# Performance work log

Measured on AMD Instinct MI355X. Metric: run time of the kernel, lower is better.

Reference implementation:

```python
import jax, jax.numpy as jnp
import numpy as np

N_HEAD = 16
N_EMBD = 1024
B, T = 4, 1024


def setup_inputs() -> dict:
    key = jax.random.key(0)
    ks = jax.random.split(key, 8)
    hs = N_EMBD // N_HEAD
    x = jax.random.normal(ks[0], (B, T, N_EMBD), dtype=jnp.float32)
    # previous-layer attention load per token, ~O(1/T) like a softmax column mean
    refractory_state = jax.random.uniform(ks[1], (B, T), dtype=jnp.float32) / T
    s_attn = 1.0 / np.sqrt(N_EMBD)
    W_attn = jax.random.normal(ks[2], (N_EMBD, 3 * N_EMBD), dtype=jnp.float32) * s_attn
    b_attn = jnp.zeros((3 * N_EMBD,), dtype=jnp.float32)
    W_proj = jax.random.normal(ks[3], (N_EMBD, N_EMBD), dtype=jnp.float32) * s_attn
    b_proj = jnp.zeros((N_EMBD,), dtype=jnp.float32)
    # learnable LIF params, init per module (lif_mode='refractory')
    threshold = jnp.full((N_HEAD,), 0.01, dtype=jnp.float32)
    leak = jnp.full((N_HEAD,), 2.0, dtype=jnp.float32)
    steepness = jnp.full((N_HEAD,), 2.0, dtype=jnp.float32)
    ref_strength = jnp.full((N_HEAD,), -2.0, dtype=jnp.float32)
    cross_w = jnp.full((N_HEAD,), -2.0, dtype=jnp.float32)
    return {
        "x": x, "refractory_state": refractory_state,
        "W_attn": W_attn, "b_attn": b_attn,
        "W_proj": W_proj, "b_proj": b_proj,
        "threshold": threshold, "leak": leak, "steepness": steepness,
        "ref_strength": ref_strength, "cross_w": cross_w,
    }


def reference(x, refractory_state, W_attn, b_attn, W_proj, b_proj,
              threshold, leak, steepness, ref_strength, cross_w):
    Bq, Tq, C = x.shape
    H = N_HEAD
    hs = C // H
    qkv = x @ W_attn + b_attn                     # [B,T,3C]
    q, k, v = jnp.split(qkv, 3, axis=-1)
    q = q.reshape(Bq, Tq, H, hs).transpose(0, 2, 1, 3)  # [B,H,T,hs]
    k = k.reshape(Bq, Tq, H, hs).transpose(0, 2, 1, 3)
    v = v.reshape(Bq, Tq, H, hs).transpose(0, 2, 1, 3)

    att = jnp.einsum('bhqd,bhkd->bhqk', q, k) * (1.0 / jnp.sqrt(jnp.asarray(hs, x.dtype)))
    causal = jnp.tril(jnp.ones((Tq, Tq), dtype=bool))
    att = jnp.where(causal[None, None], att, -jnp.inf)
    probs = jax.nn.softmax(att, axis=-1)          # [B,H,T,T]

    thr = (jnp.abs(threshold) * 0.1)[None, :, None, None]
    lk = jax.nn.sigmoid(leak)[None, :, None, None]
    st = jax.nn.softplus(steepness)[None, :, None, None]
    # refractory: column load over queries + cross-layer load
    column_load = probs.mean(axis=-2, keepdims=True)          # [B,H,1,T]
    eff_thr = thr + jax.nn.softplus(ref_strength)[None, :, None, None] * column_load
    eff_thr = eff_thr + jax.nn.sigmoid(cross_w)[None, :, None, None] * refractory_state[:, None, None, :]

    fire = jax.nn.sigmoid(st * (probs - eff_thr))
    lif_w = fire + lk * (1.0 - fire)
    mod = probs * lif_w
    mod = mod / (mod.sum(axis=-1, keepdims=True) + 1e-8)
    new_refractory = mod.mean(axis=1).mean(axis=-2)           # [B,T]

    y = jnp.einsum('bhqk,bhkd->bhqd', mod, v)
    y = y.transpose(0, 2, 1, 3).reshape(Bq, Tq, C)
    y = y @ W_proj + b_proj
    return y, new_refractory
```

## Files before the change

kernel.cpp:

```cpp
#include <hip/hip_runtime.h>
#include <math.h>

#define B_  4
#define T_  1024
#define C_  1024
#define H_  16
#define HS_ 64
#define K2E 0.1803368801f
#define LOG2E 1.44269504f

typedef _Float16 f16;
typedef _Float16 f16x8 __attribute__((ext_vector_type(8)));
typedef _Float16 f16x4 __attribute__((ext_vector_type(4)));
typedef float f32x4 __attribute__((ext_vector_type(4)));

#define MFMA16(a,b,c) __builtin_amdgcn_mfma_f32_16x16x32_f16(a,b,c,0,0,0)
#define EXP2(x) __builtin_amdgcn_exp2f(x)
#define RCP(x)  __builtin_amdgcn_rcpf(x)

#define PSTRIDE_BH 557056

__device__ __forceinline__ float qsum_(float v){
    v += __shfl_xor(v,1,64); v += __shfl_xor(v,2,64);
    v += __shfl_xor(v,4,64); v += __shfl_xor(v,8,64);
    return v;
}
__device__ __forceinline__ float sigmoidf_(float x){ return 1.0f/(1.0f + __expf(-x)); }
__device__ __forceinline__ float softplusf_(float x){ return fmaxf(x, 0.0f) + log1pf(__expf(-fabsf(x))); }

__device__ __forceinline__ void gload_lds16(const f16* g, f16* l){
    __builtin_amdgcn_global_load_lds(
        (__attribute__((address_space(1))) void*)(void*)g,
        (__attribute__((address_space(3))) void*)(void*)l, 16, 0, 0);
}

__global__ __launch_bounds__(256) void prep_k(
    const float* __restrict__ x, const float* __restrict__ Wa,
    const float* __restrict__ Wp,
    f16* __restrict__ x_h, f16* __restrict__ WaT, f16* __restrict__ WpT,
    float* __restrict__ zbase)
{
    __shared__ float tl[32][33];
    const int bid = blockIdx.x, tid = threadIdx.x;
    if (bid < 2048){
        int i = bid*256 + tid;
        const float4* p = (const float4*)x + (size_t)i*2;
        float4 a = p[0], b = p[1];
        f16x8 o;
        o[0]=(f16)a.x; o[1]=(f16)a.y; o[2]=(f16)a.z; o[3]=(f16)a.w;
        o[4]=(f16)b.x; o[5]=(f16)b.y; o[6]=(f16)b.z; o[7]=(f16)b.w;
        *((f16x8*)x_h + i) = o;
    } else if (bid < 5120){
        int t = bid - 2048;
        int n0 = (t % 96)*32, k0 = (t / 96)*32;
        const int c = tid & 31, r4 = tid >> 5;
        #pragma unroll
        for (int i=0;i<4;i++){ int r = r4*4+i; tl[r][c] = Wa[(size_t)(k0+r)*3072 + n0 + c]; }
        __syncthreads();
        #pragma unroll
        for (int i=0;i<4;i++){ int r = r4*4+i; WaT[(size_t)(n0+r)*1024 + k0 + c] = (f16)tl[c][r]; }
    } else if (bid < 6144){
        int t = bid - 5120;
        int n0 = (t & 31)*32, k0 = (t >> 5)*32;
        const int c = tid & 31, r4 = tid >> 5;
        #pragma unroll
        for (int i=0;i<4;i++){ int r = r4*4+i; tl[r][c] = Wp[(size_t)(k0+r)*1024 + n0 + c]; }
        __syncthreads();
        #pragma unroll
        for (int i=0;i<4;i++){ int r = r4*4+i; WpT[(size_t)(n0+r)*1024 + k0 + c] = (f16)tl[c][r]; }
    } else {
        int idx = (bid - 6144)*256 + tid;
        float4 z; z.x=0.f; z.y=0.f; z.z=0.f; z.w=0.f;
        ((float4*)zbase)[idx] = z;
    }
}

#define CT_STRIDE  132
#define CTV_STRIDE 136
__global__ __launch_bounds__(256) void gemm_qkv_k(
    const f16* __restrict__ A, const f16* __restrict__ Bt,
    const float* __restrict__ bias,
    f16* __restrict__ Qh, f16* __restrict__ Kh, f16* __restrict__ Vt)
{
    __shared__ __align__(16) f16 smem[17408];
    const int tid = threadIdx.x;
    const int lane = tid & 63, wave = tid >> 6;
    const int lx = lane & 15, quad = lane >> 4;
    const int wm = wave & 1, wn = wave >> 1;
    const int lin = blockIdx.y*24 + blockIdx.x;
    const int nb  = (lin & 7)*96 + (lin >> 3);
    const int m0 = (nb/24)*128, n0 = (nb%24)*128;
    const f16* Ap = A  + (size_t)m0*1024;
    const f16* Bp = Bt + (size_t)n0*1024;
    f32x4 acc[4][4];
    #pragma unroll
    for (int i=0;i<4;i++){
        #pragma unroll
        for (int j=0;j<4;j++){ acc[i][j][0]=0.f;acc[i][j][1]=0.f;acc[i][j][2]=0.f;acc[i][j][3]=0.f; }
    }
#define GQ_STAGE(BUF, KT) { \
    const int k0s = (KT)*32; \
    for (int i=0;i<2;i++){ int c=i*4+wave; \
        gload_lds16(Ap + (size_t)(c*16+lx)*1024 + k0s + quad*8, &smem[(BUF) + c*512]); \
        gload_lds16(Bp + (size_t)(c*16+lx)*1024 + k0s + quad*8, &smem[(BUF) + 4096 + c*512]); } }
#define GQ_COMP(BUF) { \
    f16x8 af[4], bf[4]; \
    for (int mt=0;mt<4;mt++) af[mt] = *(const f16x8*)&smem[(BUF) + (wm*4+mt)*512 + quad*128 + lx*8]; \
    for (int nt=0;nt<4;nt++) bf[nt] = *(const f16x8*)&smem[(BUF) + 4096 + (wn*4+nt)*512 + quad*128 + lx*8]; \
    for (int mt=0;mt<4;mt++) \
        for (int nt=0;nt<4;nt++) \
            acc[mt][nt] = MFMA16(af[mt], bf[nt], acc[mt][nt]); }

    GQ_STAGE(0, 0);
    __syncthreads();
    #pragma unroll 1
    for (int it=0; it<32; it+=2){
        if (it+1 < 32) GQ_STAGE(8192, it+1);
        GQ_COMP(0);
        __syncthreads();
        if (it+2 < 32) GQ_STAGE(0, it+2);
        GQ_COMP(8192);
        __syncthreads();
    }
    f16* Ct = smem;
    const bool isV = (n0 >= 2048);
    if (!isV){
        #pragma unroll
        for (int mt=0;mt<4;mt++){
            #pragma unroll
            for (int nt=0;nt<4;nt++){
                int n_loc = wn*64 + nt*16 + lx;
                float bv = bias[n0 + n_loc];
                #pragma unroll
                for (int r=0;r<4;r++){
                    int m_loc = wm*64 + mt*16 + quad*4 + r;
                    Ct[m_loc*CT_STRIDE + n_loc] = (f16)(acc[mt][nt][r] + bv);
                }
            }
        }
    } else {
        #pragma unroll
        for (int mt=0;mt<4;mt++){
            #pragma unroll
            for (int nt=0;nt<4;nt++){
                int n_loc = wn*64 + nt*16 + lx;
                float bv = bias[n0 + n_loc];
                int m_base = wm*64 + mt*16 + quad*4;
                f16x4 t4;
                #pragma unroll
                for (int r=0;r<4;r++) t4[r] = (f16)(acc[mt][nt][r] + bv);
                *(f16x4*)&Ct[n_loc*CTV_STRIDE + m_base] = t4;
            }
        }
    }
    __syncthreads();
    const int bb = m0 >> 10;
    if (!isV){
        for (int it=0; it<8; it++){
            int row = it*32 + wave*8 + (lane>>3);
            int ch  = lane & 7;
            int m_loc = row >> 1, half = row & 1;
            f16x8 v = *(const f16x8*)&Ct[m_loc*CT_STRIDE + half*64 + ch*8];
            int n = n0 + half*64;
            int which = n >> 10, cc = n & 1023, h = cc >> 6;
            int t = (m0 + m_loc) & 1023;
            f16* dst = (which==0) ? Qh : Kh;
            *(f16x8*)(dst + ((size_t)(bb*16+h)*1024 + t)*64 + ch*8) = v;
        }
    } else {
        for (int it=0; it<8; it++){
            int drow = it*16 + wave*4 + (lane>>4);
            int ch   = lane & 15;
            f16x8 v = *(const f16x8*)&Ct[drow*CTV_STRIDE + ch*8];
            int cc = (n0 + drow) & 1023;
            int h = cc >> 6, d = cc & 63;
            int t = (m0 + ch*8) & 1023;
            *(f16x8*)(Vt + ((size_t)(bb*16+h)*64 + d)*1024 + t) = v;
        }
    }
}

__global__ __launch_bounds__(256) void gemm_proj_k(
    const f16* __restrict__ A, const f16* __restrict__ Bt,
    const float* __restrict__ bias, float* __restrict__ out,
    const float* __restrict__ racc)
{
    if (blockIdx.x == 512){
        float* oref = out + (size_t)B_*T_*C_;
        #pragma unroll
        for (int j=0;j<16;j++){
            int idx = j*256 + threadIdx.x;
            oref[idx] = racc[idx] * (1.0f/(H_*T_));
        }
        return;
    }
    __shared__ __align__(16) f16 smem[12288];
    const int tid = threadIdx.x;
    const int lane = tid & 63, wave = tid >> 6;
    const int lx = lane & 15, quad = lane >> 4;
    const int wm = wave & 1, wn = wave >> 1;
    const int lin = blockIdx.x;
    const int nb  = (lin & 7)*64 + (lin >> 3);
    const int m0 = (nb >> 4)*128, n0 = (nb & 15)*64;
    const f16* Ap = A  + (size_t)m0*1024;
    const f16* Bp = Bt + (size_t)n0*1024;
    f32x4 acc[4][2];
    #pragma unroll
    for (int i=0;i<4;i++){
        #pragma unroll
        for (int j=0;j<2;j++){ acc[i][j][0]=0.f;acc[i][j][1]=0.f;acc[i][j][2]=0.f;acc[i][j][3]=0.f; }
    }
#define GP_STAGE(BUF, KT) { \
    const int k0s = (KT)*32; \
    for (int i=0;i<2;i++){ int c=i*4+wave; \
        gload_lds16(Ap + (size_t)(c*16+lx)*1024 + k0s + quad*8, &smem[(BUF) + c*512]); } \
    gload_lds16(Bp + (size_t)(wave*16+lx)*1024 + k0s + quad*8, &smem[(BUF) + 4096 + wave*512]); }
#define GP_COMP(BUF) { \
    f16x8 af[4], bf[2]; \
    for (int mt=0;mt<4;mt++) af[mt] = *(const f16x8*)&smem[(BUF) + (wm*4+mt)*512 + quad*128 + lx*8]; \
    for (int nt=0;nt<2;nt++) bf[nt] = *(const f16x8*)&smem[(BUF) + 4096 + (wn*2+nt)*512 + quad*128 + lx*8]; \
    for (int mt=0;mt<4;mt++) \
        for (int nt=0;nt<2;nt++) \
            acc[mt][nt] = MFMA16(af[mt], bf[nt], acc[mt][nt]); }

    GP_STAGE(0, 0);
    __syncthreads();
    #pragma unroll 1
    for (int it=0; it<32; it+=2){
        if (it+1 < 32) GP_STAGE(6144, it+1);
        GP_COMP(0);
        __syncthreads();
        if (it+2 < 32) GP_STAGE(0, it+2);
        GP_COMP(6144);
        __syncthreads();
    }
    #pragma unroll
    for (int mt=0;mt<4;mt++){
        #pragma unroll
        for (int nt=0;nt<2;nt++){
            int n = n0 + wn*32 + nt*16 + lx;
            float bv = bias[n];
            #pragma unroll
            for (int r=0;r<4;r++){
                int m = m0 + wm*64 + mt*16 + quad*4 + r;
                out[(size_t)m*1024 + n] = acc[mt][nt][r] + bv;
            }
        }
    }
}

__global__ __launch_bounds__(256) void attn_stats_k(
    const f16* __restrict__ Qh, const f16* __restrict__ Kh,
    float* __restrict__ rowl, float* __restrict__ colp,
    f16* __restrict__ Pbuf)
{
    __shared__ __align__(16) f16 Kl[8192];
    __shared__ __align__(16) f16 Pl[4][16*72];
    __shared__ float invl_sh[64];
    const int tid = threadIdx.x;
    const int lane = tid & 63, wave = tid >> 6;
    const int lx = lane & 15, quad = lane >> 4;
    const int g  = 15 - (blockIdx.x >> 6);
    const int bh = blockIdx.x & 63;
    const int qpos = wave*16 + quad*4;
    const size_t kbase = (size_t)bh*65536;
    const int S = (g+1)*64;
    f16* __restrict__ Pblk = Pbuf + (size_t)bh*PSTRIDE_BH + (size_t)4096*((g*(g+1))>>1);

    const size_t qoff = ((size_t)bh*1024 + g*64 + wave*16 + lx)*64;
    f16x8 aq0 = *(const f16x8*)(Qh + qoff + quad*8);
    f16x8 aq1 = *(const f16x8*)(Qh + qoff + 32 + quad*8);

#define KLOAD(dst, KT) { \
    for (int i=0;i<2;i++){ int u=i*4+wave, cc=u&3, kh=u>>2; \
        dst[i] = *(const f16x8*)(Kh + kbase + (size_t)((KT)*64 + cc*16+lx)*64 + kh*32 + quad*8); } }
#define KSTORE(src, BUF) { \
    for (int i=0;i<2;i++){ int u=i*4+wave, cc=u&3, kh=u>>2; \
        *(f16x8*)&Kl[(BUF) + cc*1024 + kh*512 + quad*128 + lx*8] = src[i]; } }
#define STATS1_TILE(KT, BUF) { \
    const bool diag = ((KT) == g); \
    for (int nt=0;nt<4;nt++){ \
        f32x4 sc = {0.f,0.f,0.f,0.f}; \
        f16x8 b0 = *(const f16x8*)&Kl[(BUF) + nt*1024 + quad*128 + lx*8]; \
        f16x8 b1 = *(const f16x8*)&Kl[(BUF) + nt*1024 + 512 + quad*128 + lx*8]; \
        sc = MFMA16(aq0, b0, sc); \
        sc = MFMA16(aq1, b1, sc); \
        for (int r=0;r<4;r++){ \
            float sv = sc[r]; \
            if (diag && (nt*16+lx) > (qpos + r)) sv = -1e4f; \
            float p = EXP2(sv*K2E); \
            ls[r] += p; \
            Pl[wave][(quad*4+r)*72 + nt*16 + lx] = (f16)p; \
        } } \
    for (int it2=0; it2<2; it2++){ \
        int qq = it2*8 + (lane>>3), chh = lane & 7; \
        f16x8 v = *(const f16x8*)&Pl[wave][qq*72 + chh*8]; \
        *(f16x8*)(Pblk + (size_t)(wave*16+qq)*S + (KT)*64 + chh*8) = v; } }

    f16x8 rkE[2], rkO[2];
    float ls[4] = {0.f,0.f,0.f,0.f};
    KLOAD(rkE, 0);
    KSTORE(rkE, 0);
    if (g >= 1) KLOAD(rkO, 1);
    __syncthreads();
    #pragma unroll 1
    for (int kt=0; kt<=g; kt+=2){
        if (kt+2 <= g) KLOAD(rkE, kt+2);
        if (kt+1 <= g) KSTORE(rkO, 4096);
        STATS1_TILE(kt, 0);
        __syncthreads();
        if (kt+1 <= g){
            if (kt+3 <= g) KLOAD(rkO, kt+3);
            if (kt+2 <= g) KSTORE(rkE, 0);
            STATS1_TILE(kt+1, 4096);
            __syncthreads();
        }
    }
    #pragma unroll
    for (int r=0;r<4;r++){
        float l = qsum_(ls[r]);
        if (lx == 0){
            rowl[(size_t)bh*1024 + g*64 + qpos + r] = l;
            invl_sh[qpos + r] = RCP(l);
        }
    }
    __syncthreads();
    if (tid < (g+1)*16){
        const int k0 = tid*4;
        float a0=0.f, a1=0.f, a2=0.f, a3=0.f;
        const f16* pr = Pblk + k0;
        #pragma unroll 4
        for (int q=0;q<64;q++){
            f16x4 v = *(const f16x4*)(pr + (size_t)q*S);
            float w = invl_sh[q];
            a0 += (float)v[0]*w; a1 += (float)v[1]*w;
            a2 += (float)v[2]*w; a3 += (float)v[3]*w;
        }
        float* cp = colp + (size_t)bh*1024 + k0;
        atomicAdd(cp+0,a0); atomicAdd(cp+1,a1);
        atomicAdd(cp+2,a2); atomicAdd(cp+3,a3);
    }
}

__global__ __launch_bounds__(256) void attn_apply_k(
    const f16* __restrict__ Vt,
    const float* __restrict__ rowl,
    const float* __restrict__ colp, const float* __restrict__ refr,
    const float* __restrict__ threshold, const float* __restrict__ leak,
    const float* __restrict__ steepness, const float* __restrict__ ref_strength,
    const float* __restrict__ cross_w,
    f16* __restrict__ Yh, float* __restrict__ racc,
    f16* __restrict__ Pbuf)
{
    __shared__ __align__(16) f16 Vl[8192];
    __shared__ __align__(16) f16 Pl[4][16*72];
    __shared__ float eb[1024];
    __shared__ float invl_sh[64];
    __shared__ float invD_sh[64];
    const int tid = threadIdx.x;
    const int lane = tid & 63, wave = tid >> 6;
    const int lx = lane & 15, quad = lane >> 4;
    const int g  = 15 - (blockIdx.x >> 6);
    const int bh = blockIdx.x & 63;
    const int b  = bh >> 4, h = bh & 15;
    const size_t kbase = (size_t)bh*65536;
    const int S = (g+1)*64;
    f16* __restrict__ Pblk = Pbuf + (size_t)bh*PSTRIDE_BH + (size_t)4096*((g*(g+1))>>1);

    const float thr = fabsf(threshold[h])*0.1f;
    const float lk  = sigmoidf_(leak[h]);
    const float st2 = softplusf_(steepness[h]) * LOG2E;
    const float sprT= softplusf_(ref_strength[h]) * (1.0f/T_);
    const float cw  = sigmoidf_(cross_w[h]);
    const float Alk = 1.f - lk;

    {
        float4 cp = *(const float4*)(colp + (size_t)bh*1024 + tid*4);
        float4 rf = *(const float4*)(refr + (size_t)b*1024 + tid*4);
        eb[tid*4+0] = st2*(thr + sprT*cp.x + cw*rf.x);
        eb[tid*4+1] = st2*(thr + sprT*cp.y + cw*rf.y);
        eb[tid*4+2] = st2*(thr + sprT*cp.z + cw*rf.z);
        eb[tid*4+3] = st2*(thr + sprT*cp.w + cw*rf.w);
    }
    if (tid < 64) invl_sh[tid] = RCP(rowl[(size_t)bh*1024 + g*64 + tid]);
    __syncthreads();

    const float wli = invl_sh[wave*16 + lx];

    f32x4 y[4];
    #pragma unroll
    for (int i=0;i<4;i++){ y[i][0]=0.f;y[i][1]=0.f;y[i][2]=0.f;y[i][3]=0.f; }
    float Dp = 0.f;

#define VLOAD(dst, KT) { \
    for (int i=0;i<2;i++){ int u=i*4+wave, cc=u&3, kh=u>>2; \
        dst[i] = *(const f16x8*)(Vt + kbase + (size_t)(cc*16+lx)*1024 + (KT)*64 + kh*32 + quad*8); } }
#define VSTORE(src, BUF) { \
    for (int i=0;i<2;i++){ int u=i*4+wave, cc=u&3, kh=u>>2; \
        *(f16x8*)&Vl[(BUF) + cc*1024 + kh*512 + quad*128 + lx*8] = src[i]; } }
#define PLOADX(dst, KT) { \
    const f16* pp = Pblk + (size_t)(wave*16 + lx)*S + (KT)*64 + quad*8; \
    dst[0] = *(const f16x8*)(pp); \
    dst[1] = *(const f16x8*)(pp + 32); }
#define APPLY_T(KT, BUF, pv) { \
    const float* ebp = &eb[(KT)*64 + quad*8]; \
    float4 eA0 = *(const float4*)(ebp); \
    float4 eA1 = *(const float4*)(ebp+4); \
    float4 eB0 = *(const float4*)(ebp+32); \
    float4 eB1 = *(const float4*)(ebp+36); \
    float ea[8] = {eA0.x,eA0.y,eA0.z,eA0.w,eA1.x,eA1.y,eA1.z,eA1.w}; \
    float ebb[8] = {eB0.x,eB0.y,eB0.z,eB0.w,eB1.x,eB1.y,eB1.z,eB1.w}; \
    f16x8 af0, af1; \
    for (int jj=0;jj<8;jj++){ \
        float p = (float)pv[0][jj] * wli; \
        float fire = RCP(1.f + EXP2(ea[jj] - st2*p)); \
        float pw = p*(lk + Alk*fire); \
        Dp += pw; af0[jj] = (f16)pw; } \
    for (int jj=0;jj<8;jj++){ \
        float p = (float)pv[1][jj] * wli; \
        float fire = RCP(1.f + EXP2(ebb[jj] - st2*p)); \
        float pw = p*(lk + Alk*fire); \
        Dp += pw; af1[jj] = (f16)pw; } \
    for (int dt=0;dt<4;dt++){ \
        f16x8 bv0 = *(const f16x8*)&Vl[(BUF) + dt*1024 + quad*128 + lx*8]; \
        f16x8 bv1 = *(const f16x8*)&Vl[(BUF) + dt*1024 + 512 + quad*128 + lx*8]; \
        y[dt] = MFMA16(af0, bv0, y[dt]); \
        y[dt] = MFMA16(af1, bv1, y[dt]); } }

    f16x8 rvE[2], rvO[2], pvE[2], pvO[2];
    VLOAD(rvE, 0); PLOADX(pvE, 0);
    VSTORE(rvE, 0);
    if (g >= 1){ VLOAD(rvO, 1); PLOADX(pvO, 1); }
    __syncthreads();
    #pragma unroll 1
    for (int kt=0; kt<=g; kt+=2){
        if (kt+2 <= g) VLOAD(rvE, kt+2);
        if (kt+1 <= g) VSTORE(rvO, 4096);
        APPLY_T(kt, 0, pvE);
        if (kt+2 <= g) PLOADX(pvE, kt+2);
        __syncthreads();
        if (kt+1 <= g){
            if (kt+3 <= g) VLOAD(rvO, kt+3);
            if (kt+2 <= g) VSTORE(rvE, 0);
            APPLY_T(kt+1, 4096, pvO);
            if (kt+3 <= g) PLOADX(pvO, kt+3);
            __syncthreads();
        }
    }
    Dp += __shfl_xor(Dp,16,64); Dp += __shfl_xor(Dp,32,64);
    if (quad == 0) invD_sh[wave*16 + lx] = RCP(Dp + 1e-8f);

    float invD[4];
    #pragma unroll
    for (int r=0;r<4;r++) invD[r] = invD_sh[wave*16 + quad*4 + r];
    #pragma unroll
    for (int dt=0;dt<4;dt++){
        #pragma unroll
        for (int r=0;r<4;r++)
            Pl[wave][(quad*4+r)*72 + dt*16 + lx] = (f16)(y[dt][r]*invD[r]);
    }
    #pragma unroll
    for (int it=0; it<2; it++){
        int q = it*8 + (lane>>3), ch = lane & 7;
        f16x8 v = *(const f16x8*)&Pl[wave][q*72 + ch*8];
        *(f16x8*)(Yh + (size_t)(b*1024 + g*64 + wave*16 + q)*1024 + h*64 + ch*8) = v;
    }

    __syncthreads();

    if (tid < (g+1)*16){
        const int k0 = tid*4;
        float4 ebv = *(const float4*)&eb[k0];
        float a0=0.f, a1=0.f, a2=0.f, a3=0.f;
        const f16* pr = Pblk + k0;
        #pragma unroll 4
        for (int q=0;q<64;q++){
            f16x4 v = *(const f16x4*)(pr + (size_t)q*S);
            float wl = invl_sh[q], wd = invD_sh[q];
            float p0 = (float)v[0]*wl, p1 = (float)v[1]*wl;
            float p2 = (float)v[2]*wl, p3 = (float)v[3]*wl;
            float f0 = RCP(1.f + EXP2(ebv.x - st2*p0));
            float f1 = RCP(1.f + EXP2(ebv.y - st2*p1));
            float f2 = RCP(1.f + EXP2(ebv.z - st2*p2));
            float f3 = RCP(1.f + EXP2(ebv.w - st2*p3));
            a0 += p0*(lk + Alk*f0)*wd; a1 += p1*(lk + Alk*f1)*wd;
            a2 += p2*(lk + Alk*f2)*wd; a3 += p3*(lk + Alk*f3)*wd;
        }
        float* rp = racc + (size_t)b*1024 + k0;
        atomicAdd(rp+0,a0); atomicAdd(rp+1,a1);
        atomicAdd(rp+2,a2); atomicAdd(rp+3,a3);
    }
}

extern "C" void kernel_launch(void* const* d_in, const int* in_sizes, int n_in,
                              void* d_out, int out_size, void* d_ws, size_t ws_size,
                              hipStream_t stream) {
    (void)in_sizes; (void)n_in; (void)out_size; (void)ws_size;
    const float* x           = (const float*)d_in[0];
    const float* refr        = (const float*)d_in[1];
    const float* W_attn      = (const float*)d_in[2];
    const float* b_attn      = (const float*)d_in[3];
    const float* W_proj      = (const float*)d_in[4];
    const float* b_proj      = (const float*)d_in[5];
    const float* threshold   = (const float*)d_in[6];
    const float* leak        = (const float*)d_in[7];
    const float* steepness   = (const float*)d_in[8];
    const float* ref_strength= (const float*)d_in[9];
    const float* cross_w     = (const float*)d_in[10];
    float* out = (float*)d_out;

    char* ws = (char*)d_ws;
    f16* x_h = (f16*)ws;                       ws += (size_t)4096*1024*2;
    f16* WaT = (f16*)ws;                       ws += (size_t)3072*1024*2;
    f16* WpT = (f16*)ws;                       ws += (size_t)1024*1024*2;
    f16* Qh  = (f16*)ws;                       ws += (size_t)64*1024*64*2;
    f16* Kh  = (f16*)ws;                       ws += (size_t)64*1024*64*2;
    f16* Vt  = (f16*)ws;                       ws += (size_t)64*64*1024*2;
    f16* Yh  = (f16*)ws;                       ws += (size_t)4096*1024*2;
    float* rowl = (float*)ws;                  ws += (size_t)65536*4;
    float* colp = (float*)ws;                  ws += (size_t)65536*4;
    float* racc = (float*)ws;                  ws += (size_t)4096*4;
    f16* Pbuf = (f16*)ws;                      ws += (size_t)64*PSTRIDE_BH*2;

    prep_k<<<dim3(6212), dim3(256), 0, stream>>>(x, W_attn, W_proj, x_h, WaT, WpT, colp);
    gemm_qkv_k<<<dim3(24,32), dim3(256), 0, stream>>>(x_h, WaT, b_attn, Qh, Kh, Vt);
    attn_stats_k<<<dim3(1024), dim3(256), 0, stream>>>(Qh, Kh, rowl, colp, Pbuf);
    attn_apply_k<<<dim3(1024), dim3(256), 0, stream>>>(
        Vt, rowl, colp, refr,
        threshold, leak, steepness, ref_strength, cross_w, Yh, racc, Pbuf);
    gemm_proj_k<<<dim3(513), dim3(256), 0, stream>>>(Yh, WpT, b_proj, out, racc);
}
```

Before: 258.5 us.

## Split attn_apply blocks into two 32-query halves with 128 threads each

Each attn_apply block now covers 32 query rows with 2 waves instead of 64 rows with 4 waves, and the grid doubles to 2048 blocks. The output staging buffer is aliased onto the V LDS buffer, so LDS per block shrinks and occupancy can rise. The aim is to improve load balance across the causal triangle and raise parallelism. In exchange, every block reloads the full V tiles, so V traffic doubles, and twice as many refractory atomics are issued.

```diff
diff --git a/kernel.cpp b/kernel.cpp
--- a/kernel.cpp
+++ b/kernel.cpp
@@ -342,7 +342,7 @@
     }
 }
 
-__global__ __launch_bounds__(256) void attn_apply_k(
+__global__ __launch_bounds__(128) void attn_apply_k(
     const f16* __restrict__ Vt,
     const float* __restrict__ rowl,
     const float* __restrict__ colp, const float* __restrict__ refr,
@@ -353,16 +353,18 @@
     f16* __restrict__ Pbuf)
 {
     __shared__ __align__(16) f16 Vl[8192];
-    __shared__ __align__(16) f16 Pl[4][16*72];
     __shared__ float eb[1024];
-    __shared__ float invl_sh[64];
-    __shared__ float invD_sh[64];
+    __shared__ float invl_sh[32];
+    __shared__ float invD_sh[32];
     const int tid = threadIdx.x;
     const int lane = tid & 63, wave = tid >> 6;
     const int lx = lane & 15, quad = lane >> 4;
-    const int g  = 15 - (blockIdx.x >> 6);
+    const int gq = blockIdx.x >> 6;
+    const int g  = 15 - (gq >> 1);
+    const int half = gq & 1;
     const int bh = blockIdx.x & 63;
     const int b  = bh >> 4, h = bh & 15;
+    const int q0 = half*32;
     const size_t kbase = (size_t)bh*65536;
     const int S = (g+1)*64;
     f16* __restrict__ Pblk = Pbuf + (size_t)bh*PSTRIDE_BH + (size_t)4096*((g*(g+1))>>1);
@@ -375,14 +377,18 @@
     const float Alk = 1.f - lk;
 
     {
-        float4 cp = *(const float4*)(colp + (size_t)bh*1024 + tid*4);
-        float4 rf = *(const float4*)(refr + (size_t)b*1024 + tid*4);
-        eb[tid*4+0] = st2*(thr + sprT*cp.x + cw*rf.x);
-        eb[tid*4+1] = st2*(thr + sprT*cp.y + cw*rf.y);
-        eb[tid*4+2] = st2*(thr + sprT*cp.z + cw*rf.z);
-        eb[tid*4+3] = st2*(thr + sprT*cp.w + cw*rf.w);
-    }
-    if (tid < 64) invl_sh[tid] = RCP(rowl[(size_t)bh*1024 + g*64 + tid]);
+        #pragma unroll
+        for (int s=0; s<2; s++){
+            int base = tid*8 + s*4;
+            float4 cp = *(const float4*)(colp + (size_t)bh*1024 + base);
+            float4 rf = *(const float4*)(refr + (size_t)b*1024 + base);
+            eb[base+0] = st2*(thr + sprT*cp.x + cw*rf.x);
+            eb[base+1] = st2*(thr + sprT*cp.y + cw*rf.y);
+            eb[base+2] = st2*(thr + sprT*cp.z + cw*rf.z);
+            eb[base+3] = st2*(thr + sprT*cp.w + cw*rf.w);
+        }
+    }
+    if (tid < 32) invl_sh[tid] = RCP(rowl[(size_t)bh*1024 + g*64 + q0 + tid]);
     __syncthreads();
 
     const float wli = invl_sh[wave*16 + lx];
@@ -393,13 +399,13 @@
     float Dp = 0.f;
 
 #define VLOAD(dst, KT) { \
-    for (int i=0;i<2;i++){ int u=i*4+wave, cc=u&3, kh=u>>2; \
+    for (int i=0;i<4;i++){ int u=i*2+wave, cc=u&3, kh=u>>2; \
         dst[i] = *(const f16x8*)(Vt + kbase + (size_t)(cc*16+lx)*1024 + (KT)*64 + kh*32 + quad*8); } }
 #define VSTORE(src, BUF) { \
-    for (int i=0;i<2;i++){ int u=i*4+wave, cc=u&3, kh=u>>2; \
+    for (int i=0;i<4;i++){ int u=i*2+wave, cc=u&3, kh=u>>2; \
         *(f16x8*)&Vl[(BUF) + cc*1024 + kh*512 + quad*128 + lx*8] = src[i]; } }
 #define PLOADX(dst, KT) { \
-    const f16* pp = Pblk + (size_t)(wave*16 + lx)*S + (KT)*64 + quad*8; \
+    const f16* pp = Pblk + (size_t)(q0 + wave*16 + lx)*S + (KT)*64 + quad*8; \
     dst[0] = *(const f16x8*)(pp); \
     dst[1] = *(const f16x8*)(pp + 32); }
 #define APPLY_T(KT, BUF, pv) { \
@@ -427,7 +433,7 @@
         y[dt] = MFMA16(af0, bv0, y[dt]); \
         y[dt] = MFMA16(af1, bv1, y[dt]); } }
 
-    f16x8 rvE[2], rvO[2], pvE[2], pvO[2];
+    f16x8 rvE[4], rvO[4], pvE[2], pvO[2];
     VLOAD(rvE, 0); PLOADX(pvE, 0);
     VSTORE(rvE, 0);
     if (g >= 1){ VLOAD(rvO, 1); PLOADX(pvO, 1); }
@@ -450,6 +456,7 @@
     Dp += __shfl_xor(Dp,16,64); Dp += __shfl_xor(Dp,32,64);
     if (quad == 0) invD_sh[wave*16 + lx] = RCP(Dp + 1e-8f);
 
+    f16* Plw = Vl + wave*1152;
     float invD[4];
     #pragma unroll
     for (int r=0;r<4;r++) invD[r] = invD_sh[wave*16 + quad*4 + r];
@@ -457,38 +464,38 @@
     for (int dt=0;dt<4;dt++){
         #pragma unroll
         for (int r=0;r<4;r++)
-            Pl[wave][(quad*4+r)*72 + dt*16 + lx] = (f16)(y[dt][r]*invD[r]);
+            Plw[(quad*4+r)*72 + dt*16 + lx] = (f16)(y[dt][r]*invD[r]);
     }
     #pragma unroll
     for (int it=0; it<2; it++){
         int q = it*8 + (lane>>3), ch = lane & 7;
-        f16x8 v = *(const f16x8*)&Pl[wave][q*72 + ch*8];
-        *(f16x8*)(Yh + (size_t)(b*1024 + g*64 + wave*16 + q)*1024 + h*64 + ch*8) = v;
-    }
-
-    __syncthreads();
-
-    if (tid < (g+1)*16){
-        const int k0 = tid*4;
-        float4 ebv = *(const float4*)&eb[k0];
-        float a0=0.f, a1=0.f, a2=0.f, a3=0.f;
-        const f16* pr = Pblk + k0;
+        f16x8 v = *(const f16x8*)&Plw[q*72 + ch*8];
+        *(f16x8*)(Yh + (size_t)(b*1024 + g*64 + q0 + wave*16 + q)*1024 + h*64 + ch*8) = v;
+    }
+
+    __syncthreads();
+
+    if (tid < (g+1)*8){
+        const int k0 = tid*8;
+        float4 e0 = *(const float4*)&eb[k0];
+        float4 e1 = *(const float4*)&eb[k0+4];
+        float ebv[8] = {e0.x,e0.y,e0.z,e0.w,e1.x,e1.y,e1.z,e1.w};
+        float a[8] = {0.f,0.f,0.f,0.f,0.f,0.f,0.f,0.f};
+        const f16* pr = Pblk + (size_t)q0*S + k0;
         #pragma unroll 4
-        for (int q=0;q<64;q++){
-            f16x4 v = *(const f16x4*)(pr + (size_t)q*S);
+        for (int q=0;q<32;q++){
+            f16x8 v = *(const f16x8*)(pr + (size_t)q*S);
             float wl = invl_sh[q], wd = invD_sh[q];
-            float p0 = (float)v[0]*wl, p1 = (float)v[1]*wl;
-            float p2 = (float)v[2]*wl, p3 = (float)v[3]*wl;
-            float f0 = RCP(1.f + EXP2(ebv.x - st2*p0));
-            float f1 = RCP(1.f + EXP2(ebv.y - st2*p1));
-            float f2 = RCP(1.f + EXP2(ebv.z - st2*p2));
-            float f3 = RCP(1.f + EXP2(ebv.w - st2*p3));
-            a0 += p0*(lk + Alk*f0)*wd; a1 += p1*(lk + Alk*f1)*wd;
-            a2 += p2*(lk + Alk*f2)*wd; a3 += p3*(lk + Alk*f3)*wd;
+            #pragma unroll
+            for (int j=0;j<8;j++){
+                float p = (float)v[j]*wl;
+                float f = RCP(1.f + EXP2(ebv[j] - st2*p));
+                a[j] += p*(lk + Alk*f)*wd;
+            }
         }
         float* rp = racc + (size_t)b*1024 + k0;
-        atomicAdd(rp+0,a0); atomicAdd(rp+1,a1);
-        atomicAdd(rp+2,a2); atomicAdd(rp+3,a3);
+        #pragma unroll
+        for (int j=0;j<8;j++) atomicAdd(rp+j, a[j]);
     }
 }
 
@@ -525,7 +532,7 @@
     prep_k<<<dim3(6212), dim3(256), 0, stream>>>(x, W_attn, W_proj, x_h, WaT, WpT, colp);
     gemm_qkv_k<<<dim3(24,32), dim3(256), 0, stream>>>(x_h, WaT, b_attn, Qh, Kh, Vt);
     attn_stats_k<<<dim3(1024), dim3(256), 0, stream>>>(Qh, Kh, rowl, colp, Pbuf);
-    attn_apply_k<<<dim3(1024), dim3(256), 0, stream>>>(
+    attn_apply_k<<<dim3(2048), dim3(128), 0, stream>>>(
         Vt, rowl, colp, refr,
         threshold, leak, steepness, ref_strength, cross_w, Yh, racc, Pbuf);
     gemm_proj_k<<<dim3(513), dim3(256), 0, stream>>>(Yh, WpT, b_proj, out, racc);
```

Result: slower. 345.1 us (+33.5%).
